# Kernel tuning notes

Hardware: AMD Instinct MI355X
Metric: run time of the kernel (lower is better)

The kernel has to match this reference:

```python
import jax, jax.numpy as jnp
import numpy as np

N, E, EE = 1024, 32768, 262144
C_S, C_Z, C_G, H, R = 384, 128, 16, 4, 64
EPS = 1e-8


def _rbf(d, D_count=R, D_min=0.0, D_max=20.0):
    # gvp-style radial basis: exp(-((d - mu)/sigma)^2), mu in linspace(D_min, D_max)
    mu = jnp.linspace(D_min, D_max, D_count, dtype=d.dtype)
    sigma = (D_max - D_min) / D_count
    return jnp.exp(-(((d[..., None] - mu) / sigma) ** 2))


def _layernorm(x, g, b, eps=1e-5):
    m = jnp.mean(x, axis=-1, keepdims=True)
    v = jnp.var(x, axis=-1, keepdims=True)
    return (x - m) * jax.lax.rsqrt(v + eps) * g + b


def setup_inputs() -> dict:
    key = jax.random.key(0)
    ks = jax.random.split(key, 32)
    s = 0.02
    inp = {
        'node_features': jax.random.normal(ks[0], (N, C_S), jnp.float32),
        'node_trans': jax.random.normal(ks[1], (N, 3), jnp.float32) * 10.0,
        'edge_features': jax.random.normal(ks[2], (E, C_Z), jnp.float32),
        'edge_index': jax.random.randint(ks[3], (2, E), 0, N),
        'edge_edge_index': jax.random.randint(ks[4], (2, EE), 0, E),
        # layer norm
        'ln_g': jnp.ones((C_Z,), jnp.float32),
        'ln_b': jnp.zeros((C_Z,), jnp.float32),
        # node_left / node_right
        'W_nl': jax.random.normal(ks[5], (C_S, C_G), jnp.float32) * s,
        'b_nl': jnp.zeros((C_G,), jnp.float32),
        'W_nr': jax.random.normal(ks[6], (C_S, C_G), jnp.float32) * s,
        'b_nr': jnp.zeros((C_G,), jnp.float32),
        # bias_gate: (c_gate_s^2 -> c_z)
        'W_bg': jax.random.normal(ks[7], (C_G * C_G, C_Z), jnp.float32) * s,
        'b_bg': jnp.zeros((C_Z,), jnp.float32),
        # dist_bias: (num_rbf -> c_z)
        'W_db': jax.random.normal(ks[8], (R, C_Z), jnp.float32) * s,
        'b_db': jnp.zeros((C_Z,), jnp.float32),
        # to_bias: (c_z -> num_heads), no bias
        'W_tb': jax.random.normal(ks[9], (C_Z, H), jnp.float32) * s,
        # q / kv
        'W_q': jax.random.normal(ks[10], (C_Z, C_Z), jnp.float32) * s,
        'b_q': jnp.zeros((C_Z,), jnp.float32),
        'W_kv': jax.random.normal(ks[11], (C_Z, 2 * C_Z), jnp.float32) * s,
        'b_kv': jnp.zeros((2 * C_Z,), jnp.float32),
        # out gate + out proj
        'W_og': jax.random.normal(ks[12], (C_Z, C_Z), jnp.float32) * s,
        'b_og': jnp.zeros((C_Z,), jnp.float32),
        'W_out': jax.random.normal(ks[13], (C_Z, C_Z), jnp.float32) * s,
        'b_out': jnp.zeros((C_Z,), jnp.float32),
    }
    return inp


def reference(node_features, node_trans, edge_features, edge_index, edge_edge_index,
              ln_g, ln_b, W_nl, b_nl, W_nr, b_nr, W_bg, b_bg, W_db, b_db, W_tb,
              W_q, b_q, W_kv, b_kv, W_og, b_og, W_out, b_out):
    d = C_Z // H
    ee0, ee1 = edge_edge_index[0], edge_edge_index[1]
    # node indices of the two triangle corner nodes for each edge-edge pair
    n1 = edge_index[0, ee1]  # [EE]
    n2 = edge_index[0, ee0]  # [EE]

    ef = _layernorm(edge_features, ln_g, ln_b)  # [E, c_z]

    nl = node_features @ W_nl + b_nl  # [N, c_g]
    nr = node_features @ W_nr + b_nr
    # outer product gate features per edge-edge pair
    e3 = jnp.einsum('bi,bj->bij', nl[n1], nr[n2]).reshape(-1, C_G * C_G)  # [EE, c_g^2]
    gate = e3 @ W_bg + b_bg  # [EE, c_z]

    dist = jnp.linalg.norm(node_trans[n1] - node_trans[n2] + EPS, axis=-1)  # [EE]
    dist_bias = _rbf(dist) @ W_db + b_db  # [EE, c_z]
    bias = (jax.nn.sigmoid(gate) * dist_bias) @ W_tb  # [EE, H]

    q = (ef @ W_q + b_q).reshape(E, H, d)
    kv = ef @ W_kv + b_kv
    k = kv[:, :C_Z].reshape(E, H, d)
    v = kv[:, C_Z:].reshape(E, H, d)

    attn = jnp.einsum('bhi,bhi->bh', q[ee1], k[ee0]) * (1.0 / np.sqrt(C_Z)) + bias  # [EE, H]

    # segment softmax over target edge ee1
    seg_max = jax.ops.segment_max(attn, ee1, num_segments=E)  # [E, H]
    p = jnp.exp(attn - seg_max[ee1])
    seg_sum = jax.ops.segment_sum(p, ee1, num_segments=E)
    p = p / (seg_sum[ee1] + 1e-16)

    upd = jax.ops.segment_sum(v[ee0] * p[..., None], ee1, num_segments=E)  # [E, H, d]
    upd = upd.reshape(E, C_Z)
    upd = upd * jax.nn.sigmoid(ef @ W_og + b_og)
    return upd @ W_out + b_out
```

## Files before the change

kernel.cpp:

```cpp
#include <hip/hip_runtime.h>
#include <math.h>

#define NN 1024
#define NE 32768
#define NEE 262144
#define CS 384
#define CZ 128
#define CG 16
#define NH 4
#define NR 64

typedef __attribute__((ext_vector_type(8))) short short8v;
typedef __attribute__((ext_vector_type(4))) float f32x4;
typedef unsigned short ushort_t;

__device__ __forceinline__ float sigmoidf_(float x) { return 1.0f / (1.0f + __expf(-x)); }

__device__ __forceinline__ ushort_t f2bf(float x) {
    union { float f; unsigned u; } v; v.f = x;
    unsigned r = v.u + 0x7fff + ((v.u >> 16) & 1);
    return (ushort_t)(r >> 16);
}
__device__ __forceinline__ float bf2f(ushort_t x) {
    union { unsigned u; float f; } v; v.u = ((unsigned)x) << 16;
    return v.f;
}

__global__ void node_proj_kernel(const float* __restrict__ nf,
                                 const float* __restrict__ Wl, const float* __restrict__ bl,
                                 const float* __restrict__ Wr, const float* __restrict__ br,
                                 ushort_t* __restrict__ nl16, float* __restrict__ nr) {
    int wave = threadIdx.x >> 6, lane = threadIdx.x & 63;
    int n = blockIdx.x * 4 + wave;
    if (lane >= 32) return;
    bool isl = lane < 16;
    int o = isl ? lane : lane - 16;
    const float* W = isl ? Wl : Wr;
    float acc = isl ? bl[o] : br[o];
    const float* x = nf + n * CS;
    for (int k = 0; k < CS; ++k) acc += x[k] * W[k * 16 + o];
    if (isl) nl16[n * 16 + o] = f2bf(acc);
    else     nr[n * 16 + o] = acc;
}

__global__ void build_Tt_kernel(const float* __restrict__ nr, const float* __restrict__ Wbg,
                                ushort_t* __restrict__ Tbf) {
    int n = blockIdx.x;
    int t = threadIdx.x;
    int c = t & 127, i0 = t >> 7;
    __shared__ float nrs[16];
    if (t < 16) nrs[t] = nr[n * 16 + t];
    __syncthreads();
    for (int i = i0; i < 16; i += 2) {
        float acc = 0.f;
#pragma unroll
        for (int j = 0; j < 16; ++j) acc += nrs[j] * Wbg[(i * 16 + j) * 128 + c];
        Tbf[n * 2048 + c * 16 + i] = f2bf(acc);
    }
}

__global__ void ln_kernel(const float* __restrict__ x, const float* __restrict__ g,
                          const float* __restrict__ b, ushort_t* __restrict__ ef) {
    int wave = threadIdx.x >> 6, lane = threadIdx.x & 63;
    int e = blockIdx.x * 4 + wave;
    int c0 = lane, c1 = lane + 64;
    float x0 = x[e * 128 + c0], x1 = x[e * 128 + c1];
    float s = x0 + x1;
#pragma unroll
    for (int m = 1; m < 64; m <<= 1) s += __shfl_xor(s, m);
    float mean = s * (1.f / 128.f);
    float d0 = x0 - mean, d1 = x1 - mean;
    float v = d0 * d0 + d1 * d1;
#pragma unroll
    for (int m = 1; m < 64; m <<= 1) v += __shfl_xor(v, m);
    v *= (1.f / 128.f);
    float inv = rsqrtf(v + 1e-5f);
    ef[e * 128 + c0] = f2bf(d0 * inv * g[c0] + b[c0]);
    ef[e * 128 + c1] = f2bf(d1 * inv * g[c1] + b[c1]);
}

__global__ void prep_w_kernel(const float* __restrict__ Wq, const float* __restrict__ bq,
                              const float* __restrict__ Wkv, const float* __restrict__ bkv,
                              const float* __restrict__ Wog, const float* __restrict__ bog,
                              const float* __restrict__ Wdb, const float* __restrict__ Wout,
                              ushort_t* __restrict__ WcatT, float* __restrict__ bcat,
                              ushort_t* __restrict__ WdbT, ushort_t* __restrict__ WoutT) {
    int idx = blockIdx.x * 256 + threadIdx.x;
    int col = idx >> 7, k = idx & 127;
    float w;
    if (col < 128) w = Wq[k * 128 + col];
    else if (col < 256) w = Wog[k * 128 + (col - 128)];
    else if (col < 384) w = Wkv[k * 256 + (col - 256)];
    else w = Wkv[k * 256 + 128 + (col - 384)];
    WcatT[idx] = f2bf(w);
    if (idx < 512) {
        float bb;
        if (idx < 128) bb = bq[idx];
        else if (idx < 256) bb = bog[idx - 128];
        else if (idx < 384) bb = bkv[idx - 256];
        else bb = bkv[idx - 384 + 128];
        bcat[idx] = bb;
    }
    if (idx < 128 * 64) {
        int c = idx >> 6, r = idx & 63;
        WdbT[idx] = f2bf(Wdb[r * 128 + c]);
    }
    if (idx < 128 * 128) {
        int c = idx >> 7, kk = idx & 127;
        WoutT[idx] = f2bf(Wout[kk * 128 + c]);
    }
}

__global__ void __launch_bounds__(256) mfma_gemm_proj(const ushort_t* __restrict__ Abf,
                                                      const ushort_t* __restrict__ Bt,
                                                      const float* __restrict__ bias,
                                                      ushort_t* __restrict__ qog,
                                                      ushort_t* __restrict__ kvo) {
    __shared__ ushort_t As[128][136];
    __shared__ ushort_t Bs[64][136];
    int t = threadIdx.x;
    int row0 = blockIdx.y * 128;
    int n0 = blockIdx.x * 64;
#pragma unroll
    for (int u = 0; u < 8; ++u) {
        int idx = t + u * 256;
        int r = idx >> 4, seg = idx & 15;
        *(short8v*)&As[r][seg * 8] = *(const short8v*)&Abf[(size_t)(row0 + r) * 128 + seg * 8];
    }
#pragma unroll
    for (int u = 0; u < 4; ++u) {
        int idx = t + u * 256;
        int r = idx >> 4, seg = idx & 15;
        *(short8v*)&Bs[r][seg * 8] = *(const short8v*)&Bt[(size_t)(n0 + r) * 128 + seg * 8];
    }
    __syncthreads();
    int lane = t & 63, w = t >> 6;
    int wr = (w >> 1) * 64, wc = (w & 1) * 32;
    int fr = lane & 15, fk = (lane >> 4) * 8;
    f32x4 acc[4][2] = {};
#pragma unroll
    for (int kk = 0; kk < 4; ++kk) {
        short8v a[4], b[2];
#pragma unroll
        for (int m = 0; m < 4; ++m) a[m] = *(const short8v*)&As[wr + m * 16 + fr][kk * 32 + fk];
#pragma unroll
        for (int n = 0; n < 2; ++n) b[n] = *(const short8v*)&Bs[wc + n * 16 + fr][kk * 32 + fk];
#pragma unroll
        for (int m = 0; m < 4; ++m)
#pragma unroll
            for (int n = 0; n < 2; ++n)
                acc[m][n] = __builtin_amdgcn_mfma_f32_16x16x32_bf16(a[m], b[n], acc[m][n], 0, 0, 0);
    }
    __syncthreads();
    ushort_t (*stage)[72] = (ushort_t(*)[72])&As[0][0];
    int orow = (lane >> 4) * 4;
#pragma unroll
    for (int m = 0; m < 4; ++m)
#pragma unroll
        for (int n = 0; n < 2; ++n) {
            int col = wc + n * 16 + fr;
            float bv = bias[n0 + col];
#pragma unroll
            for (int j = 0; j < 4; ++j)
                stage[wr + m * 16 + orow + j][col] = f2bf(acc[m][n][j] + bv);
        }
    __syncthreads();
    ushort_t* basep; int cbase;
    if (n0 < 256) { basep = qog; cbase = n0; } else { basep = kvo; cbase = n0 - 256; }
#pragma unroll
    for (int u = 0; u < 4; ++u) {
        int idx = t + u * 256;
        int r = idx >> 3, seg = idx & 7;
        *(short8v*)&basep[(size_t)(row0 + r) * 256 + cbase + seg * 8] = *(const short8v*)&stage[r][seg * 8];
    }
}

__global__ void __launch_bounds__(256) mfma_gemm_out(const float* __restrict__ Af,
                                                     const ushort_t* __restrict__ Bt,
                                                     const float* __restrict__ bias,
                                                     float* __restrict__ out) {
    __shared__ ushort_t As[128][136];
    __shared__ ushort_t Bs[64][136];
    int t = threadIdx.x;
    int row0 = blockIdx.y * 128;
    int n0 = blockIdx.x * 64;
#pragma unroll
    for (int u = 0; u < 8; ++u) {
        int idx = t + u * 256;
        int r = idx >> 4, seg = idx & 15;
        float4 f0 = *(const float4*)&Af[(size_t)(row0 + r) * 128 + seg * 8];
        float4 f1 = *(const float4*)&Af[(size_t)(row0 + r) * 128 + seg * 8 + 4];
        short8v pk;
        pk[0] = (short)f2bf(f0.x); pk[1] = (short)f2bf(f0.y);
        pk[2] = (short)f2bf(f0.z); pk[3] = (short)f2bf(f0.w);
        pk[4] = (short)f2bf(f1.x); pk[5] = (short)f2bf(f1.y);
        pk[6] = (short)f2bf(f1.z); pk[7] = (short)f2bf(f1.w);
        *(short8v*)&As[r][seg * 8] = pk;
    }
#pragma unroll
    for (int u = 0; u < 4; ++u) {
        int idx = t + u * 256;
        int r = idx >> 4, seg = idx & 15;
        *(short8v*)&Bs[r][seg * 8] = *(const short8v*)&Bt[(size_t)(n0 + r) * 128 + seg * 8];
    }
    __syncthreads();
    int lane = t & 63, w = t >> 6;
    int wr = (w >> 1) * 64, wc = (w & 1) * 32;
    int fr = lane & 15, fk = (lane >> 4) * 8;
    f32x4 acc[4][2] = {};
#pragma unroll
    for (int kk = 0; kk < 4; ++kk) {
        short8v a[4], b[2];
#pragma unroll
        for (int m = 0; m < 4; ++m) a[m] = *(const short8v*)&As[wr + m * 16 + fr][kk * 32 + fk];
#pragma unroll
        for (int n = 0; n < 2; ++n) b[n] = *(const short8v*)&Bs[wc + n * 16 + fr][kk * 32 + fk];
#pragma unroll
        for (int m = 0; m < 4; ++m)
#pragma unroll
            for (int n = 0; n < 2; ++n)
                acc[m][n] = __builtin_amdgcn_mfma_f32_16x16x32_bf16(a[m], b[n], acc[m][n], 0, 0, 0);
    }
    __syncthreads();
    float (*stage)[68] = (float(*)[68])&As[0][0];
    int orow = (lane >> 4) * 4;
#pragma unroll
    for (int m = 0; m < 4; ++m)
#pragma unroll
        for (int n = 0; n < 2; ++n) {
            int col = wc + n * 16 + fr;
            float bv = bias[n0 + col];
#pragma unroll
            for (int j = 0; j < 4; ++j)
                stage[wr + m * 16 + orow + j][col] = acc[m][n][j] + bv;
        }
    __syncthreads();
#pragma unroll
    for (int u = 0; u < 8; ++u) {
        int idx = t + u * 256;
        int r = idx >> 4, c4 = idx & 15;
        *(float4*)&out[(size_t)(row0 + r) * 128 + n0 + c4 * 4] = *(const float4*)&stage[r][c4 * 4];
    }
}

__global__ void hist_kernel(const int* __restrict__ eei, const int* __restrict__ ei,
                            int* __restrict__ cnt, int* __restrict__ cnt2) {
    int p = blockIdx.x * 256 + threadIdx.x;
    int e0 = eei[p], e1 = eei[NEE + p];
    atomicAdd(&cnt[e1], 1);
    atomicAdd(&cnt2[ei[e0]], 1);
}

__global__ void scan_kernel(const int* __restrict__ cnt, int* __restrict__ offs,
                            int* __restrict__ cursor) {
    __shared__ int part[1024];
    int t = threadIdx.x;
    int loc[32];
    int s = 0;
#pragma unroll
    for (int j = 0; j < 32; ++j) { loc[j] = cnt[t * 32 + j]; s += loc[j]; }
    part[t] = s;
    __syncthreads();
    for (int d = 1; d < 1024; d <<= 1) {
        int add = (t >= d) ? part[t - d] : 0;
        __syncthreads();
        part[t] += add;
        __syncthreads();
    }
    int excl = (t == 0) ? 0 : part[t - 1];
#pragma unroll
    for (int j = 0; j < 32; ++j) {
        offs[t * 32 + j] = excl;
        cursor[t * 32 + j] = excl;
        excl += loc[j];
    }
    if (t == 1023) offs[NE] = excl;
}

__global__ void scan2_kernel(const int* __restrict__ cnt2, int* __restrict__ offs2,
                             int* __restrict__ cursor2) {
    __shared__ int part[256];
    int t = threadIdx.x;
    int loc[4];
    int s = 0;
#pragma unroll
    for (int j = 0; j < 4; ++j) { loc[j] = cnt2[t * 4 + j]; s += loc[j]; }
    part[t] = s;
    __syncthreads();
    for (int d = 1; d < 256; d <<= 1) {
        int add = (t >= d) ? part[t - d] : 0;
        __syncthreads();
        part[t] += add;
        __syncthreads();
    }
    int excl = (t == 0) ? 0 : part[t - 1];
#pragma unroll
    for (int j = 0; j < 4; ++j) {
        offs2[t * 4 + j] = excl;
        cursor2[t * 4 + j] = excl;
        excl += loc[j];
    }
    if (t == 255) offs2[1024] = excl;
}

__global__ void scatter_both_kernel(const int* __restrict__ eei, const int* __restrict__ ei,
                                    const float* __restrict__ ntr,
                                    int* __restrict__ cursor, int* __restrict__ csr,
                                    int* __restrict__ cursor2, int* __restrict__ csr2,
                                    int* __restrict__ n1rank, float* __restrict__ drank) {
    int p = blockIdx.x * 256 + threadIdx.x;
    int e0 = eei[p], e1 = eei[NEE + p];
    int pos = atomicAdd(&cursor[e1], 1);
    csr[pos] = p;
    int n1 = ei[e1], n2 = ei[e0];
    int pos2 = atomicAdd(&cursor2[n2], 1);
    csr2[pos2] = p;
    n1rank[pos2] = n1;
    float dx = ntr[n1 * 3 + 0] - ntr[n2 * 3 + 0] + 1e-8f;
    float dy = ntr[n1 * 3 + 1] - ntr[n2 * 3 + 1] + 1e-8f;
    float dz = ntr[n1 * 3 + 2] - ntr[n2 * 3 + 2] + 1e-8f;
    drank[pos2] = sqrtf(dx * dx + dy * dy + dz * dz);
}

#define BSPLIT 4
__global__ void __launch_bounds__(256) bias_kernel(
    const int* __restrict__ csr2, const int* __restrict__ offs2,
    const int* __restrict__ n1rank, const float* __restrict__ drank,
    const ushort_t* __restrict__ nl16, const ushort_t* __restrict__ Tbf,
    const ushort_t* __restrict__ WdbT,
    const float* __restrict__ bbg, const float* __restrict__ bdb,
    const float* __restrict__ Wtb, float* __restrict__ bias_p) {
    __shared__ ushort_t Tt[128 * 24];
    __shared__ ushort_t Wd[128 * 72];
    int t = threadIdx.x;
    int n2 = blockIdx.x >> 2;
    int s  = blockIdx.x & 3;
    {
        const ushort_t* src = Tbf + n2 * 2048;
        int c = t >> 1, hh = t & 1;
        *(int4*)&Tt[c * 24 + hh * 8] = *(const int4*)&src[c * 16 + hh * 8];
    }
#pragma unroll
    for (int u = 0; u < 4; ++u) {
        int idx = t + u * 256;
        int c = idx >> 3, seg = idx & 7;
        *(int4*)&Wd[c * 72 + seg * 8] = *(const int4*)&WdbT[c * 64 + seg * 8];
    }
    __syncthreads();

    int lane = t & 63, w = t >> 6;
    int cl = lane & 15, g = lane >> 4;
    float wtb[8][4], bdbl[8], bbgl[8];
#pragma unroll
    for (int nb = 0; nb < 8; ++nb) {
        int c = nb * 16 + cl;
        float4 wt = *(const float4*)&Wtb[c * 4];
        wtb[nb][0] = wt.x; wtb[nb][1] = wt.y; wtb[nb][2] = wt.z; wtb[nb][3] = wt.w;
        bdbl[nb] = bdb[c];
        bbgl[nb] = bbg[c];
    }
    int bstart = offs2[n2], bend = offs2[n2 + 1];
    const float MU = 20.0f / 63.0f;

    for (int base = bstart + (s * 4 + w) * 16; base < bend; base += 16 * 4 * BSPLIT) {
        int idx = base + cl;
        int ip = (idx < bend) ? idx : (bend - 1);
        int n1 = n1rank[ip];
        float d = drank[ip];
        short8v aNL = {0, 0, 0, 0, 0, 0, 0, 0};
        if (g < 2) aNL = *(const short8v*)&nl16[n1 * 16 + g * 8];
        short8v ea, eb;
#pragma unroll
        for (int j = 0; j < 8; ++j) {
            float r = (float)(g * 8 + j);
            float t0 = (d - r * MU) * 3.2f;
            float t1 = (d - (r + 32.0f) * MU) * 3.2f;
            ea[j] = (short)f2bf(__expf(-t0 * t0));
            eb[j] = (short)f2bf(__expf(-t1 * t1));
        }
        float bacc[4][4] = {};
        f32x4 zero4 = {0.f, 0.f, 0.f, 0.f};
#pragma unroll
        for (int nb = 0; nb < 8; ++nb) {
            int c = nb * 16 + cl;
            short8v bT = {0, 0, 0, 0, 0, 0, 0, 0};
            if (g < 2) bT = *(const short8v*)&Tt[c * 24 + g * 8];
            f32x4 G = __builtin_amdgcn_mfma_f32_16x16x32_bf16(aNL, bT, zero4, 0, 0, 0);
            short8v bW0 = *(const short8v*)&Wd[c * 72 + g * 8];
            short8v bW1 = *(const short8v*)&Wd[c * 72 + 32 + g * 8];
            f32x4 D = __builtin_amdgcn_mfma_f32_16x16x32_bf16(ea, bW0, zero4, 0, 0, 0);
            D = __builtin_amdgcn_mfma_f32_16x16x32_bf16(eb, bW1, D, 0, 0, 0);
#pragma unroll
            for (int j = 0; j < 4; ++j) {
                float gv = G[j] + bbgl[nb];
                float db = D[j] + bdbl[nb];
                float sg = db * sigmoidf_(gv);
                bacc[j][0] += sg * wtb[nb][0];
                bacc[j][1] += sg * wtb[nb][1];
                bacc[j][2] += sg * wtb[nb][2];
                bacc[j][3] += sg * wtb[nb][3];
            }
        }
#pragma unroll
        for (int j = 0; j < 4; ++j)
#pragma unroll
            for (int h = 0; h < 4; ++h) {
                float v = bacc[j][h];
                v += __shfl_xor(v, 1);
                v += __shfl_xor(v, 2);
                v += __shfl_xor(v, 4);
                v += __shfl_xor(v, 8);
                bacc[j][h] = v;
            }
        int row = g * 4 + (cl >> 2), h = cl & 3;
        int oidx = base + row;
        if (oidx < bend) {
            int pp = csr2[oidx];
            bias_p[pp * 4 + h] = bacc[cl >> 2][h];
        }
    }
}

__global__ void __launch_bounds__(256) segment_kernel(const ushort_t* __restrict__ qog,
                                                      const ushort_t* __restrict__ kv,
                                                      const float* __restrict__ bias_p,
                                                      const int* __restrict__ offs,
                                                      const int* __restrict__ csr,
                                                      const int* __restrict__ eei,
                                                      float* __restrict__ updg) {
    int t = threadIdx.x, wave = t >> 6, lane = t & 63;
    int gw = blockIdx.x * 4 + wave;
    int h = lane >> 4;
    const float scale = 0.08838834764831845f;
    for (int it = 0; it < 4; ++it) {
        int e = gw * 4 + it;
        int st = offs[e], en = offs[e + 1];
        unsigned qw = *(const unsigned*)&qog[(size_t)e * 256 + 2 * lane];
        float q0 = bf2f((ushort_t)(qw & 0xffff)), q1 = bf2f((ushort_t)(qw >> 16));
        float s = 0.f, u0 = 0.f, u1 = 0.f;
        for (int idx = st; idx < en; ++idx) {
            int p = csr[idx];
            int e0 = eei[p];
            const ushort_t* kvr = kv + (size_t)e0 * 256;
            unsigned kw = *(const unsigned*)&kvr[2 * lane];
            unsigned vw = *(const unsigned*)&kvr[128 + 2 * lane];
            float ta = q0 * bf2f((ushort_t)(kw & 0xffff)) + q1 * bf2f((ushort_t)(kw >> 16));
#pragma unroll
            for (int m = 1; m < 16; m <<= 1) ta += __shfl_xor(ta, m);
            float wgt = __expf(ta * scale + bias_p[p * 4 + h]);
            s += wgt;
            u0 += wgt * bf2f((ushort_t)(vw & 0xffff));
            u1 += wgt * bf2f((ushort_t)(vw >> 16));
        }
        float inv = 1.0f / (s + 1e-16f);
        unsigned ogw = *(const unsigned*)&qog[(size_t)e * 256 + 128 + 2 * lane];
        u0 = u0 * inv * sigmoidf_(bf2f((ushort_t)(ogw & 0xffff)));
        u1 = u1 * inv * sigmoidf_(bf2f((ushort_t)(ogw >> 16)));
        float2 uo; uo.x = u0; uo.y = u1;
        *(float2*)&updg[(size_t)e * 128 + 2 * lane] = uo;
    }
}

extern "C" void kernel_launch(void* const* d_in, const int* in_sizes, int n_in,
                              void* d_out, int out_size, void* d_ws, size_t ws_size,
                              hipStream_t stream) {
    const float* node_features = (const float*)d_in[0];
    const float* node_trans   = (const float*)d_in[1];
    const float* edge_features= (const float*)d_in[2];
    const int*   edge_index   = (const int*)d_in[3];
    const int*   eei          = (const int*)d_in[4];
    const float* ln_g  = (const float*)d_in[5];
    const float* ln_b  = (const float*)d_in[6];
    const float* W_nl  = (const float*)d_in[7];
    const float* b_nl  = (const float*)d_in[8];
    const float* W_nr  = (const float*)d_in[9];
    const float* b_nr  = (const float*)d_in[10];
    const float* W_bg  = (const float*)d_in[11];
    const float* b_bg  = (const float*)d_in[12];
    const float* W_db  = (const float*)d_in[13];
    const float* b_db  = (const float*)d_in[14];
    const float* W_tb  = (const float*)d_in[15];
    const float* W_q   = (const float*)d_in[16];
    const float* b_q   = (const float*)d_in[17];
    const float* W_kv  = (const float*)d_in[18];
    const float* b_kv  = (const float*)d_in[19];
    const float* W_og  = (const float*)d_in[20];
    const float* b_og  = (const float*)d_in[21];
    const float* W_out = (const float*)d_in[22];
    const float* b_out = (const float*)d_in[23];
    float* out = (float*)d_out;

    char* ws = (char*)d_ws;
    size_t off = 0;
    auto alloc = [&](size_t bytes) -> void* {
        void* p = ws + off;
        off += (bytes + 255) & ~(size_t)255;
        return p;
    };
    ushort_t* nl16  = (ushort_t*)alloc((size_t)NN * 16 * 2);
    float*    nr    = (float*)alloc((size_t)NN * 16 * 4);
    ushort_t* Tbf   = (ushort_t*)alloc((size_t)NN * 2048 * 2);
    ushort_t* WdbT  = (ushort_t*)alloc((size_t)128 * 64 * 2);
    ushort_t* WcatT = (ushort_t*)alloc((size_t)512 * 128 * 2);
    float*    bcat  = (float*)alloc((size_t)512 * 4);
    ushort_t* WoutT = (ushort_t*)alloc((size_t)128 * 128 * 2);
    ushort_t* ef_bf = (ushort_t*)alloc((size_t)NE * 128 * 2);
    ushort_t* qog   = (ushort_t*)alloc((size_t)NE * 256 * 2);
    ushort_t* kvb   = (ushort_t*)alloc((size_t)NE * 256 * 2);
    float*    bias_p= (float*)alloc((size_t)NEE * 4 * 4);
    float*    updg  = (float*)alloc((size_t)NE * 128 * 4);
    int*      cnt   = (int*)alloc((size_t)NE * 4);
    int*      cnt2  = (int*)alloc((size_t)1024 * 4);
    int*      offs  = (int*)alloc((size_t)(NE + 1) * 4);
    int*      offs2 = (int*)alloc((size_t)1025 * 4);
    int*      cursor  = (int*)alloc((size_t)NE * 4);
    int*      cursor2 = (int*)alloc((size_t)1024 * 4);
    int*      csr   = (int*)alloc((size_t)NEE * 4);
    int*      csr2  = (int*)alloc((size_t)NEE * 4);
    int*      n1rank= (int*)alloc((size_t)NEE * 4);
    float*    drank = (float*)alloc((size_t)NEE * 4);

    hipMemsetAsync(cnt, 0, (size_t)NE * 4 + 1024 * 4, stream);

    node_proj_kernel<<<NN / 4, 256, 0, stream>>>(node_features, W_nl, b_nl, W_nr, b_nr, nl16, nr);
    build_Tt_kernel<<<NN, 256, 0, stream>>>(nr, W_bg, Tbf);
    ln_kernel<<<NE / 4, 256, 0, stream>>>(edge_features, ln_g, ln_b, ef_bf);
    prep_w_kernel<<<256, 256, 0, stream>>>(W_q, b_q, W_kv, b_kv, W_og, b_og, W_db, W_out,
                                           WcatT, bcat, WdbT, WoutT);
    mfma_gemm_proj<<<dim3(8, 256), 256, 0, stream>>>(ef_bf, WcatT, bcat, qog, kvb);
    hist_kernel<<<NEE / 256, 256, 0, stream>>>(eei, edge_index, cnt, cnt2);
    scan_kernel<<<1, 1024, 0, stream>>>(cnt, offs, cursor);
    scan2_kernel<<<1, 256, 0, stream>>>(cnt2, offs2, cursor2);
    scatter_both_kernel<<<NEE / 256, 256, 0, stream>>>(eei, edge_index, node_trans,
                                                       cursor, csr, cursor2, csr2, n1rank, drank);
    bias_kernel<<<NN * BSPLIT, 256, 0, stream>>>(csr2, offs2, n1rank, drank, nl16, Tbf, WdbT,
                                                 b_bg, b_db, W_tb, bias_p);
    segment_kernel<<<NE / 16, 256, 0, stream>>>(qog, kvb, bias_p, offs, csr, eei, updg);
    mfma_gemm_out<<<dim3(2, 256), 256, 0, stream>>>(updg, WoutT, b_out, out);
}
```

Before: 452.3 us.

## Store bias in target-edge CSR order and drop double indirection in segment kernel

The scatter kernel now records e0 directly in the e1-sorted CSR order, plus a map from node-sorted position to edge-sorted position. The bias kernel writes its output straight into that edge-sorted order, so the segment kernel reads e0 and bias contiguously instead of chasing csr→eei and gathering bias by pair id. The bias kernel also drops BSPLIT, going from 4 blocks per node to 1, and reorders its MFMAs so they issue back to back before the epilogue. This reduces grid parallelism for the bias stage and raises register pressure from holding G/D arrays.

```diff
diff --git a/kernel.cpp b/kernel.cpp
--- a/kernel.cpp
+++ b/kernel.cpp
@@ -305,36 +305,34 @@
 
 __global__ void scatter_both_kernel(const int* __restrict__ eei, const int* __restrict__ ei,
                                     const float* __restrict__ ntr,
-                                    int* __restrict__ cursor, int* __restrict__ csr,
-                                    int* __restrict__ cursor2, int* __restrict__ csr2,
-                                    int* __restrict__ n1rank, float* __restrict__ drank) {
+                                    int* __restrict__ cursor, int* __restrict__ e0rank,
+                                    int* __restrict__ cursor2, int* __restrict__ n1rank,
+                                    float* __restrict__ drank, int* __restrict__ x2to1) {
     int p = blockIdx.x * 256 + threadIdx.x;
     int e0 = eei[p], e1 = eei[NEE + p];
     int pos = atomicAdd(&cursor[e1], 1);
-    csr[pos] = p;
+    e0rank[pos] = e0;
     int n1 = ei[e1], n2 = ei[e0];
     int pos2 = atomicAdd(&cursor2[n2], 1);
-    csr2[pos2] = p;
     n1rank[pos2] = n1;
+    x2to1[pos2] = pos;
     float dx = ntr[n1 * 3 + 0] - ntr[n2 * 3 + 0] + 1e-8f;
     float dy = ntr[n1 * 3 + 1] - ntr[n2 * 3 + 1] + 1e-8f;
     float dz = ntr[n1 * 3 + 2] - ntr[n2 * 3 + 2] + 1e-8f;
     drank[pos2] = sqrtf(dx * dx + dy * dy + dz * dz);
 }
 
-#define BSPLIT 4
 __global__ void __launch_bounds__(256) bias_kernel(
-    const int* __restrict__ csr2, const int* __restrict__ offs2,
-    const int* __restrict__ n1rank, const float* __restrict__ drank,
+    const int* __restrict__ offs2, const int* __restrict__ n1rank,
+    const float* __restrict__ drank, const int* __restrict__ x2to1,
     const ushort_t* __restrict__ nl16, const ushort_t* __restrict__ Tbf,
     const ushort_t* __restrict__ WdbT,
     const float* __restrict__ bbg, const float* __restrict__ bdb,
-    const float* __restrict__ Wtb, float* __restrict__ bias_p) {
+    const float* __restrict__ Wtb, float* __restrict__ bias_cs) {
     __shared__ ushort_t Tt[128 * 24];
     __shared__ ushort_t Wd[128 * 72];
     int t = threadIdx.x;
-    int n2 = blockIdx.x >> 2;
-    int s  = blockIdx.x & 3;
+    int n2 = blockIdx.x;
     {
         const ushort_t* src = Tbf + n2 * 2048;
         int c = t >> 1, hh = t & 1;
@@ -361,8 +359,9 @@
     }
     int bstart = offs2[n2], bend = offs2[n2 + 1];
     const float MU = 20.0f / 63.0f;
-
-    for (int base = bstart + (s * 4 + w) * 16; base < bend; base += 16 * 4 * BSPLIT) {
+    f32x4 zero4 = {0.f, 0.f, 0.f, 0.f};
+
+    for (int base = bstart + w * 16; base < bend; base += 64) {
         int idx = base + cl;
         int ip = (idx < bend) ? idx : (bend - 1);
         int n1 = n1rank[ip];
@@ -378,22 +377,27 @@
             ea[j] = (short)f2bf(__expf(-t0 * t0));
             eb[j] = (short)f2bf(__expf(-t1 * t1));
         }
+        f32x4 G[8], D[8];
+#pragma unroll
+        for (int nb = 0; nb < 8; ++nb) {
+            short8v bT = {0, 0, 0, 0, 0, 0, 0, 0};
+            if (g < 2) bT = *(const short8v*)&Tt[(nb * 16 + cl) * 24 + g * 8];
+            G[nb] = __builtin_amdgcn_mfma_f32_16x16x32_bf16(aNL, bT, zero4, 0, 0, 0);
+        }
+#pragma unroll
+        for (int nb = 0; nb < 8; ++nb) {
+            short8v bW0 = *(const short8v*)&Wd[(nb * 16 + cl) * 72 + g * 8];
+            short8v bW1 = *(const short8v*)&Wd[(nb * 16 + cl) * 72 + 32 + g * 8];
+            f32x4 tmp = __builtin_amdgcn_mfma_f32_16x16x32_bf16(ea, bW0, zero4, 0, 0, 0);
+            D[nb] = __builtin_amdgcn_mfma_f32_16x16x32_bf16(eb, bW1, tmp, 0, 0, 0);
+        }
         float bacc[4][4] = {};
-        f32x4 zero4 = {0.f, 0.f, 0.f, 0.f};
 #pragma unroll
         for (int nb = 0; nb < 8; ++nb) {
-            int c = nb * 16 + cl;
-            short8v bT = {0, 0, 0, 0, 0, 0, 0, 0};
-            if (g < 2) bT = *(const short8v*)&Tt[c * 24 + g * 8];
-            f32x4 G = __builtin_amdgcn_mfma_f32_16x16x32_bf16(aNL, bT, zero4, 0, 0, 0);
-            short8v bW0 = *(const short8v*)&Wd[c * 72 + g * 8];
-            short8v bW1 = *(const short8v*)&Wd[c * 72 + 32 + g * 8];
-            f32x4 D = __builtin_amdgcn_mfma_f32_16x16x32_bf16(ea, bW0, zero4, 0, 0, 0);
-            D = __builtin_amdgcn_mfma_f32_16x16x32_bf16(eb, bW1, D, 0, 0, 0);
 #pragma unroll
             for (int j = 0; j < 4; ++j) {
-                float gv = G[j] + bbgl[nb];
-                float db = D[j] + bdbl[nb];
+                float gv = G[nb][j] + bbgl[nb];
+                float db = D[nb][j] + bdbl[nb];
                 float sg = db * sigmoidf_(gv);
                 bacc[j][0] += sg * wtb[nb][0];
                 bacc[j][1] += sg * wtb[nb][1];
@@ -415,18 +419,17 @@
         int row = g * 4 + (cl >> 2), h = cl & 3;
         int oidx = base + row;
         if (oidx < bend) {
-            int pp = csr2[oidx];
-            bias_p[pp * 4 + h] = bacc[cl >> 2][h];
+            int dst = x2to1[oidx];
+            bias_cs[(size_t)dst * 4 + h] = bacc[cl >> 2][h];
         }
     }
 }
 
 __global__ void __launch_bounds__(256) segment_kernel(const ushort_t* __restrict__ qog,
                                                       const ushort_t* __restrict__ kv,
-                                                      const float* __restrict__ bias_p,
+                                                      const float* __restrict__ bias_cs,
                                                       const int* __restrict__ offs,
-                                                      const int* __restrict__ csr,
-                                                      const int* __restrict__ eei,
+                                                      const int* __restrict__ e0rank,
                                                       float* __restrict__ updg) {
     int t = threadIdx.x, wave = t >> 6, lane = t & 63;
     int gw = blockIdx.x * 4 + wave;
@@ -439,15 +442,14 @@
         float q0 = bf2f((ushort_t)(qw & 0xffff)), q1 = bf2f((ushort_t)(qw >> 16));
         float s = 0.f, u0 = 0.f, u1 = 0.f;
         for (int idx = st; idx < en; ++idx) {
-            int p = csr[idx];
-            int e0 = eei[p];
+            int e0 = e0rank[idx];
             const ushort_t* kvr = kv + (size_t)e0 * 256;
             unsigned kw = *(const unsigned*)&kvr[2 * lane];
             unsigned vw = *(const unsigned*)&kvr[128 + 2 * lane];
             float ta = q0 * bf2f((ushort_t)(kw & 0xffff)) + q1 * bf2f((ushort_t)(kw >> 16));
 #pragma unroll
             for (int m = 1; m < 16; m <<= 1) ta += __shfl_xor(ta, m);
-            float wgt = __expf(ta * scale + bias_p[p * 4 + h]);
+            float wgt = __expf(ta * scale + bias_cs[(size_t)idx * 4 + h]);
             s += wgt;
             u0 += wgt * bf2f((ushort_t)(vw & 0xffff));
             u1 += wgt * bf2f((ushort_t)(vw >> 16));
@@ -507,7 +509,7 @@
     ushort_t* ef_bf = (ushort_t*)alloc((size_t)NE * 128 * 2);
     ushort_t* qog   = (ushort_t*)alloc((size_t)NE * 256 * 2);
     ushort_t* kvb   = (ushort_t*)alloc((size_t)NE * 256 * 2);
-    float*    bias_p= (float*)alloc((size_t)NEE * 4 * 4);
+    float*    bias_cs = (float*)alloc((size_t)NEE * 4 * 4);
     float*    updg  = (float*)alloc((size_t)NE * 128 * 4);
     int*      cnt   = (int*)alloc((size_t)NE * 4);
     int*      cnt2  = (int*)alloc((size_t)1024 * 4);
@@ -515,10 +517,10 @@
     int*      offs2 = (int*)alloc((size_t)1025 * 4);
     int*      cursor  = (int*)alloc((size_t)NE * 4);
     int*      cursor2 = (int*)alloc((size_t)1024 * 4);
-    int*      csr   = (int*)alloc((size_t)NEE * 4);
-    int*      csr2  = (int*)alloc((size_t)NEE * 4);
+    int*      e0rank= (int*)alloc((size_t)NEE * 4);
     int*      n1rank= (int*)alloc((size_t)NEE * 4);
     float*    drank = (float*)alloc((size_t)NEE * 4);
+    int*      x2to1 = (int*)alloc((size_t)NEE * 4);
 
     hipMemsetAsync(cnt, 0, (size_t)NE * 4 + 1024 * 4, stream);
 
@@ -532,9 +534,9 @@
     scan_kernel<<<1, 1024, 0, stream>>>(cnt, offs, cursor);
     scan2_kernel<<<1, 256, 0, stream>>>(cnt2, offs2, cursor2);
     scatter_both_kernel<<<NEE / 256, 256, 0, stream>>>(eei, edge_index, node_trans,
-                                                       cursor, csr, cursor2, csr2, n1rank, drank);
-    bias_kernel<<<NN * BSPLIT, 256, 0, stream>>>(csr2, offs2, n1rank, drank, nl16, Tbf, WdbT,
-                                                 b_bg, b_db, W_tb, bias_p);
-    segment_kernel<<<NE / 16, 256, 0, stream>>>(qog, kvb, bias_p, offs, csr, eei, updg);
+                                                       cursor, e0rank, cursor2, n1rank, drank, x2to1);
+    bias_kernel<<<NN, 256, 0, stream>>>(offs2, n1rank, drank, x2to1, nl16, Tbf, WdbT,
+                                        b_bg, b_db, W_tb, bias_cs);
+    segment_kernel<<<NE / 16, 256, 0, stream>>>(qog, kvb, bias_cs, offs, e0rank, updg);
     mfma_gemm_out<<<dim3(2, 256), 256, 0, stream>>>(updg, WoutT, b_out, out);
 }
```

Measured after the change: 441.1 us. 1.03x faster.
